# Kernel optimization log

Measured on AMD Instinct MI355X. Metric: run time of the kernel, lower is better.

## Reference

```python
import jax, jax.numpy as jnp
import numpy as np

HEADS = 8
HEAD_DIM = 64
GROUPS = 32
EPS = 1e-5


def setup_inputs() -> dict:
    key = jax.random.key(0)
    ks = jax.random.split(key, 8)
    B, C, H, W = 16, 256, 32, 32
    TD = 1024
    inner = HEADS * HEAD_DIM
    return {
        "x": jax.random.normal(ks[0], (B, C, H, W), jnp.float32),
        "embedding": jax.random.normal(ks[1], (B, TD), jnp.float32),
        "norm_w": jnp.ones((C,), jnp.float32),
        "norm_b": jnp.zeros((C,), jnp.float32),
        "in_w": jax.random.normal(ks[2], (3 * inner, C), jnp.float32) * (1.0 / np.sqrt(C)),
        "in_b": jnp.zeros((3 * inner,), jnp.float32),
        "out_w": jax.random.normal(ks[3], (C, inner), jnp.float32) * (1.0 / np.sqrt(inner)),
        "out_b": jnp.zeros((C,), jnp.float32),
        "emb_w": jax.random.normal(ks[4], (C, TD), jnp.float32) * (1.0 / np.sqrt(TD)),
        "emb_b": jnp.zeros((C,), jnp.float32),
    }


def reference(x, embedding, norm_w, norm_b, in_w, in_b, out_w, out_b, emb_w, emb_b):
    b, c, h, w = x.shape
    scale = 1.0 / np.sqrt(HEAD_DIM)
    # GroupNorm over (C//G, H, W) per group
    xg = x.reshape(b, GROUPS, -1)
    mean = xg.mean(-1, keepdims=True)
    var = xg.var(-1, keepdims=True)
    xn = ((xg - mean) * jax.lax.rsqrt(var + EPS)).reshape(b, c, h, w)
    xn = xn * norm_w[:, None, None] + norm_b[:, None, None]
    # 1x1 conv QKV projection: [b, 3*inner, h, w]
    qkv = jnp.einsum('oc,bchw->bohw', in_w, xn) + in_b[:, None, None]
    q, k, v = jnp.split(qkv, 3, axis=1)
    # [b, heads, head_dim, hw]
    q = q.reshape(b, HEADS, HEAD_DIM, h * w)
    k = k.reshape(b, HEADS, HEAD_DIM, h * w)
    v = v.reshape(b, HEADS, HEAD_DIM, h * w)
    attn = jax.nn.softmax(jnp.einsum('bhcm,bhcn->bhmn', q, k) * scale, axis=-1)
    o = jnp.einsum('bhmn,bhcn->bhcm', attn, v)  # [b,h,c,hw]
    o = o.reshape(b, HEADS * HEAD_DIM, h, w)
    out = jnp.einsum('oc,bchw->bohw', out_w, o) + out_b[:, None, None]
    emb = embedding @ emb_w.T + emb_b  # [b, C]
    return out * emb[:, :, None, None] + x
```

## Files before the change

### kernel.cpp

```cpp
#include <hip/hip_runtime.h>

#define DEV __device__ __forceinline__

typedef _Float16 f16;
typedef _Float16 f16x8 __attribute__((ext_vector_type(8)));
typedef _Float16 f16x4 __attribute__((ext_vector_type(4)));
typedef float f32x4 __attribute__((ext_vector_type(4)));

static constexpr int NB = 16;
static constexpr int NC = 256;
static constexpr int HW = 1024;
static constexpr int NG = 32;
static constexpr int CPG = 8;
static constexpr int NH = 8;
static constexpr int HD = 64;
static constexpr int INNER = 512;
static constexpr int TD = 1024;

DEV f32x4 mfma16(f16x8 a, f16x8 b, f32x4 c) {
    return __builtin_amdgcn_mfma_f32_16x16x32_f16(a, b, c, 0, 0, 0);
}

__global__ void gn_stats_k(const float* __restrict__ x, float* __restrict__ stats) {
    int bg = blockIdx.x;
    const float4* p = reinterpret_cast<const float4*>(x) + (size_t)bg * (CPG * HW / 4);
    float s = 0.f, ss = 0.f;
    for (int i = threadIdx.x; i < CPG * HW / 4; i += 256) {
        float4 v = p[i];
        s  += v.x + v.y + v.z + v.w;
        ss += v.x * v.x + v.y * v.y + v.z * v.z + v.w * v.w;
    }
    #pragma unroll
    for (int o = 32; o > 0; o >>= 1) {
        s  += __shfl_xor(s, o);
        ss += __shfl_xor(ss, o);
    }
    __shared__ float rs[4], rss[4];
    int wid = threadIdx.x >> 6;
    if ((threadIdx.x & 63) == 0) { rs[wid] = s; rss[wid] = ss; }
    __syncthreads();
    if (threadIdx.x == 0) {
        s  = rs[0] + rs[1] + rs[2] + rs[3];
        ss = rss[0] + rss[1] + rss[2] + rss[3];
        const float inv_n = 1.f / (float)(CPG * HW);
        float mean = s * inv_n;
        float var  = ss * inv_n - mean * mean;
        stats[bg * 2]     = mean;
        stats[bg * 2 + 1] = rsqrtf(var + 1e-5f);
    }
}

__global__ void gn_apply_k(const float* __restrict__ x, const float* __restrict__ stats,
                           const float* __restrict__ nw, const float* __restrict__ nb,
                           f16* __restrict__ xnT) {
    int b = blockIdx.y;
    int m = blockIdx.x * 256 + threadIdx.x;
    const float* xb = x + (size_t)b * NC * HW + m;
    f16* op = xnT + ((size_t)b * HW + m) * NC;
    for (int c0 = 0; c0 < NC; c0 += 4) {
        f16x4 h;
        #pragma unroll
        for (int j = 0; j < 4; ++j) {
            int c = c0 + j;
            float mean = stats[(b * NG + (c >> 3)) * 2];
            float rstd = stats[(b * NG + (c >> 3)) * 2 + 1];
            float v = xb[(size_t)c * HW];
            h[j] = (f16)(((v - mean) * rstd) * nw[c] + nb[c]);
        }
        *reinterpret_cast<f16x4*>(op + c0) = h;
    }
}

__global__ void conv_w_k(const float* __restrict__ a, const float* __restrict__ bw,
                         f16* __restrict__ wa, f16* __restrict__ wb) {
    int i = blockIdx.x * 256 + threadIdx.x;
    const int N1 = 3 * INNER * NC / 4;
    float4 v;
    f16* dst;
    if (i < N1) { v = reinterpret_cast<const float4*>(a)[i];      dst = wa + (size_t)i * 4; }
    else        { v = reinterpret_cast<const float4*>(bw)[i - N1]; dst = wb + (size_t)(i - N1) * 4; }
    f16x4 h4 = {(f16)v.x, (f16)v.y, (f16)v.z, (f16)v.w};
    *reinterpret_cast<f16x4*>(dst) = h4;
}

__global__ __launch_bounds__(256) void gemm_qkv_k(
        const f16* __restrict__ wA, const f16* __restrict__ xnT,
        const float* __restrict__ bias,
        f16* __restrict__ qT, f16* __restrict__ kT, f16* __restrict__ vv) {
    int b  = blockIdx.z;
    int o0 = blockIdx.x * 128;
    int m0 = blockIdx.y * 128;
    int wid  = threadIdx.x >> 6;
    int lane = threadIdx.x & 63;
    int wr = (wid >> 1) * 64, wc = (wid & 1) * 64;
    int lr = lane & 15, lg = lane >> 4;

    const f16* A  = wA  + (size_t)(o0 + wr + lr) * NC + lg * 8;
    const f16* Bp = xnT + ((size_t)b * HW + m0 + wc + lr) * NC + lg * 8;

    const f32x4 fzero = {0.f, 0.f, 0.f, 0.f};
    f32x4 acc[4][4];
    #pragma unroll
    for (int i = 0; i < 4; ++i) {
        #pragma unroll
        for (int j = 0; j < 4; ++j) acc[i][j] = fzero;
    }

    for (int k0 = 0; k0 < NC; k0 += 32) {
        f16x8 af[4], bf[4];
        #pragma unroll
        for (int i = 0; i < 4; ++i)
            af[i] = *reinterpret_cast<const f16x8*>(A + (size_t)i * 16 * NC + k0);
        #pragma unroll
        for (int j = 0; j < 4; ++j)
            bf[j] = *reinterpret_cast<const f16x8*>(Bp + (size_t)j * 16 * NC + k0);
        #pragma unroll
        for (int i = 0; i < 4; ++i) {
            #pragma unroll
            for (int j = 0; j < 4; ++j)
                acc[i][j] = mfma16(af[i], bf[j], acc[i][j]);
        }
    }

    #pragma unroll
    for (int i = 0; i < 4; ++i) {
        int ob = o0 + wr + i * 16 + lg * 4;
        #pragma unroll
        for (int j = 0; j < 4; ++j) {
            int m = m0 + wc + j * 16 + lr;
            float v0 = acc[i][j][0] + bias[ob];
            float v1 = acc[i][j][1] + bias[ob + 1];
            float v2 = acc[i][j][2] + bias[ob + 2];
            float v3 = acc[i][j][3] + bias[ob + 3];
            if (ob < INNER) {
                int h = ob >> 6, c = ob & 63;
                f16x4 pk = {(f16)v0, (f16)v1, (f16)v2, (f16)v3};
                *reinterpret_cast<f16x4*>(qT + (((size_t)(b * NH + h) * HW + m) * HD + c)) = pk;
            } else if (ob < 2 * INNER) {
                int oo = ob - INNER;
                int h = oo >> 6, c = oo & 63;
                f16x4 pk = {(f16)v0, (f16)v1, (f16)v2, (f16)v3};
                *reinterpret_cast<f16x4*>(kT + (((size_t)(b * NH + h) * HW + m) * HD + c)) = pk;
            } else {
                int oo = ob - 2 * INNER;
                int h = oo >> 6, c = oo & 63;
                f16* vp = vv + ((size_t)(b * NH + h) * HD + c) * HW + m;
                vp[0]      = (f16)v0;
                vp[HW]     = (f16)v1;
                vp[2 * HW] = (f16)v2;
                vp[3 * HW] = (f16)v3;
            }
        }
    }
}

__global__ void emb_gemm_k(const float* __restrict__ e, const float* __restrict__ ew,
                           const float* __restrict__ eb, float* __restrict__ embS) {
    int b = blockIdx.y;
    int co = blockIdx.x * 4 + (threadIdx.x >> 6);
    int lane = threadIdx.x & 63;
    const float4* ep = reinterpret_cast<const float4*>(e + (size_t)b * TD);
    const float4* wp = reinterpret_cast<const float4*>(ew + (size_t)co * TD);
    float s = 0.f;
    for (int t = lane; t < TD / 4; t += 64) {
        float4 a = ep[t], w = wp[t];
        s += a.x * w.x + a.y * w.y + a.z * w.z + a.w * w.w;
    }
    #pragma unroll
    for (int o = 32; o > 0; o >>= 1) s += __shfl_xor(s, o);
    if (lane == 0) embS[b * NC + co] = s + eb[co];
}

__global__ __launch_bounds__(256) void attn_k(
        const f16* __restrict__ qT, const f16* __restrict__ kT, const f16* __restrict__ vv,
        f16* __restrict__ oT) {
    int bh = blockIdx.x;
    int b = bh >> 3, h = bh & 7;
    int wid = threadIdx.x >> 6;
    int lane = threadIdx.x & 63;
    int lr = lane & 15, lg = lane >> 4;
    int mw = blockIdx.y * 256 + wid * 64;

    const f16* qp = qT + (size_t)bh * HW * HD;
    const f16* kp = kT + (size_t)bh * HW * HD;
    const f16* vp = vv + (size_t)bh * HD * HW;

    const float sl = 0.125f * 1.44269504088896f;

    __shared__ __align__(16) f16 pl[4][16][40];

    f16x8 qf[4][2];
    #pragma unroll
    for (int qt = 0; qt < 4; ++qt)
        #pragma unroll
        for (int ks2 = 0; ks2 < 2; ++ks2)
            qf[qt][ks2] = *reinterpret_cast<const f16x8*>(
                qp + (size_t)(mw + qt * 16 + lr) * HD + ks2 * 32 + lg * 8);

    const f32x4 fzero = {0.f, 0.f, 0.f, 0.f};
    f32x4 oa[4][4];
    #pragma unroll
    for (int qt = 0; qt < 4; ++qt)
        #pragma unroll
        for (int dt = 0; dt < 4; ++dt) oa[qt][dt] = fzero;
    float mr[4] = {-1e30f, -1e30f, -1e30f, -1e30f};
    float ls[4] = {0.f, 0.f, 0.f, 0.f};

    for (int n0 = 0; n0 < HW; n0 += 32) {
        f16x8 kf[2][2];
        #pragma unroll
        for (int kt = 0; kt < 2; ++kt)
            #pragma unroll
            for (int ks2 = 0; ks2 < 2; ++ks2)
                kf[kt][ks2] = *reinterpret_cast<const f16x8*>(
                    kp + (size_t)(n0 + kt * 16 + lr) * HD + ks2 * 32 + lg * 8);
        f16x8 vf[4];
        #pragma unroll
        for (int dt = 0; dt < 4; ++dt)
            vf[dt] = *reinterpret_cast<const f16x8*>(
                vp + (size_t)(dt * 16 + lr) * HW + n0 + lg * 8);

        #pragma unroll
        for (int qt = 0; qt < 4; ++qt) {
            f32x4 sc[2] = {fzero, fzero};
            __builtin_amdgcn_s_setprio(1);
            #pragma unroll
            for (int kt = 0; kt < 2; ++kt)
                #pragma unroll
                for (int ks2 = 0; ks2 < 2; ++ks2)
                    sc[kt] = mfma16(kf[kt][ks2], qf[qt][ks2], sc[kt]);
            __builtin_amdgcn_s_setprio(0);

            float a0 = fmaxf(fmaxf(sc[0][0], sc[0][1]), fmaxf(sc[0][2], sc[0][3]));
            float a1 = fmaxf(fmaxf(sc[1][0], sc[1][1]), fmaxf(sc[1][2], sc[1][3]));
            float pm = fmaxf(a0, a1) * sl;
            pm = fmaxf(pm, __shfl_xor(pm, 16));
            pm = fmaxf(pm, __shfl_xor(pm, 32));
            float mn = fmaxf(mr[qt], pm);
            float f = exp2f(mr[qt] - mn);
            mr[qt] = mn;
            ls[qt] *= f;
            #pragma unroll
            for (int dt = 0; dt < 4; ++dt) {
                #pragma unroll
                for (int r = 0; r < 4; ++r) oa[qt][dt][r] *= f;
            }
            float p[8];
            #pragma unroll
            for (int kt = 0; kt < 2; ++kt)
                #pragma unroll
                for (int r = 0; r < 4; ++r)
                    p[kt * 4 + r] = exp2f(fmaf(sc[kt][r], sl, -mn));
            float rsum = ((p[0] + p[1]) + (p[2] + p[3])) + ((p[4] + p[5]) + (p[6] + p[7]));
            rsum += __shfl_xor(rsum, 16);
            rsum += __shfl_xor(rsum, 32);
            ls[qt] += rsum;

            f16x4 w0 = {(f16)p[0], (f16)p[1], (f16)p[2], (f16)p[3]};
            f16x4 w1 = {(f16)p[4], (f16)p[5], (f16)p[6], (f16)p[7]};
            *reinterpret_cast<f16x4*>(&pl[wid][lr][lg * 4])      = w0;
            *reinterpret_cast<f16x4*>(&pl[wid][lr][16 + lg * 4]) = w1;
            f16x8 pf = *reinterpret_cast<const f16x8*>(&pl[wid][lr][lg * 8]);

            __builtin_amdgcn_s_setprio(1);
            #pragma unroll
            for (int dt = 0; dt < 4; ++dt)
                oa[qt][dt] = mfma16(vf[dt], pf, oa[qt][dt]);
            __builtin_amdgcn_s_setprio(0);
        }
    }

    #pragma unroll
    for (int qt = 0; qt < 4; ++qt) {
        float inv = 1.f / ls[qt];
        int m = mw + qt * 16 + lr;
        f16* op = oT + ((size_t)b * HW + m) * INNER + h * HD;
        #pragma unroll
        for (int dt = 0; dt < 4; ++dt) {
            f16x4 o4;
            #pragma unroll
            for (int r = 0; r < 4; ++r) o4[r] = (f16)(oa[qt][dt][r] * inv);
            *reinterpret_cast<f16x4*>(op + dt * 16 + lg * 4) = o4;
        }
    }
}

__global__ __launch_bounds__(256) void gemm_out_k(
        const f16* __restrict__ wA, const f16* __restrict__ oT,
        const float* __restrict__ bias, const float* __restrict__ embS,
        const float* __restrict__ x, float* __restrict__ out) {
    int b  = blockIdx.z;
    int o0 = blockIdx.x * 128;
    int m0 = blockIdx.y * 128;
    int wid  = threadIdx.x >> 6;
    int lane = threadIdx.x & 63;
    int wr = (wid >> 1) * 64, wc = (wid & 1) * 64;
    int lr = lane & 15, lg = lane >> 4;

    const f16* A  = wA + (size_t)(o0 + wr + lr) * INNER + lg * 8;
    const f16* Bp = oT + ((size_t)b * HW + m0 + wc + lr) * INNER + lg * 8;

    const f32x4 fzero = {0.f, 0.f, 0.f, 0.f};
    f32x4 acc[4][4];
    #pragma unroll
    for (int i = 0; i < 4; ++i) {
        #pragma unroll
        for (int j = 0; j < 4; ++j) acc[i][j] = fzero;
    }

    for (int k0 = 0; k0 < INNER; k0 += 32) {
        f16x8 af[4], bf[4];
        #pragma unroll
        for (int i = 0; i < 4; ++i)
            af[i] = *reinterpret_cast<const f16x8*>(A + (size_t)i * 16 * INNER + k0);
        #pragma unroll
        for (int j = 0; j < 4; ++j)
            bf[j] = *reinterpret_cast<const f16x8*>(Bp + (size_t)j * 16 * INNER + k0);
        #pragma unroll
        for (int i = 0; i < 4; ++i) {
            #pragma unroll
            for (int j = 0; j < 4; ++j)
                acc[i][j] = mfma16(af[i], bf[j], acc[i][j]);
        }
    }

    #pragma unroll
    for (int i = 0; i < 4; ++i) {
        int ob = o0 + wr + i * 16 + lg * 4;
        #pragma unroll
        for (int j = 0; j < 4; ++j) {
            int m = m0 + wc + j * 16 + lr;
            #pragma unroll
            for (int r = 0; r < 4; ++r) {
                int o = ob + r;
                size_t idx = ((size_t)b * NC + o) * HW + m;
                out[idx] = (acc[i][j][r] + bias[o]) * embS[b * NC + o] + x[idx];
            }
        }
    }
}

extern "C" void kernel_launch(void* const* d_in, const int* in_sizes, int n_in,
                              void* d_out, int out_size, void* d_ws, size_t ws_size,
                              hipStream_t stream) {
    const float* x     = (const float*)d_in[0];
    const float* emb   = (const float*)d_in[1];
    const float* nw    = (const float*)d_in[2];
    const float* nbi   = (const float*)d_in[3];
    const float* in_w  = (const float*)d_in[4];
    const float* in_b  = (const float*)d_in[5];
    const float* out_w = (const float*)d_in[6];
    const float* out_b = (const float*)d_in[7];
    const float* emb_w = (const float*)d_in[8];
    const float* emb_b = (const float*)d_in[9];

    char* p = (char*)d_ws;
    f16* xnT   = (f16*)p;   p += (size_t)NB * HW * NC * 2;
    f16* w_in  = (f16*)p;   p += (size_t)3 * INNER * NC * 2;
    f16* w_out = (f16*)p;   p += (size_t)NC * INNER * 2;
    float* stats = (float*)p; p += (size_t)NB * NG * 2 * 4;
    float* embS  = (float*)p; p += (size_t)NB * NC * 4;
    f16* qT = (f16*)p;      p += (size_t)NB * NH * HW * HD * 2;
    f16* kT = (f16*)p;      p += (size_t)NB * NH * HW * HD * 2;
    f16* vv = (f16*)p;      p += (size_t)NB * NH * HW * HD * 2;
    f16* oT = (f16*)p;

    gn_stats_k<<<NB * NG, 256, 0, stream>>>(x, stats);
    gn_apply_k<<<dim3(HW / 256, NB), 256, 0, stream>>>(x, stats, nw, nbi, xnT);
    conv_w_k<<<512, 256, 0, stream>>>(in_w, out_w, w_in, w_out);
    gemm_qkv_k<<<dim3(12, 8, NB), 256, 0, stream>>>(w_in, xnT, in_b, qT, kT, vv);
    emb_gemm_k<<<dim3(NC / 4, NB), 256, 0, stream>>>(emb, emb_w, emb_b, embS);
    attn_k<<<dim3(NB * NH, HW / 256), 256, 0, stream>>>(qT, kT, vv, oT);
    gemm_out_k<<<dim3(NC / 128, HW / 128, NB), 256, 0, stream>>>(w_out, oT, out_b, embS, x, (float*)d_out);
}
```

Before: 197.2 us.

## Double-buffer K/V loads, lazy softmax rescale, per-lane row sums, XCD-aware block mapping

```diff
diff --git a/kernel.cpp b/kernel.cpp
--- a/kernel.cpp
+++ b/kernel.cpp
@@ -171,108 +171,124 @@
     if (lane == 0) embS[b * NC + co] = s + eb[co];
 }
 
-__global__ __launch_bounds__(256) void attn_k(
-        const f16* __restrict__ qT, const f16* __restrict__ kT, const f16* __restrict__ vv,
-        f16* __restrict__ oT) {
-    int bh = blockIdx.x;
-    int b = bh >> 3, h = bh & 7;
-    int wid = threadIdx.x >> 6;
-    int lane = threadIdx.x & 63;
-    int lr = lane & 15, lg = lane >> 4;
-    int mw = blockIdx.y * 256 + wid * 64;
-
-    const f16* qp = qT + (size_t)bh * HW * HD;
-    const f16* kp = kT + (size_t)bh * HW * HD;
-    const f16* vp = vv + (size_t)bh * HD * HW;
-
+DEV void load_kv(const f16* __restrict__ kp, const f16* __restrict__ vp,
+                 int n0, int lr, int lg, f16x8 (&kf)[2][2], f16x8 (&vf)[4]) {
+    #pragma unroll
+    for (int kt = 0; kt < 2; ++kt)
+        #pragma unroll
+        for (int ks2 = 0; ks2 < 2; ++ks2)
+            kf[kt][ks2] = *reinterpret_cast<const f16x8*>(
+                kp + (size_t)(n0 + kt * 16 + lr) * HD + ks2 * 32 + lg * 8);
+    #pragma unroll
+    for (int dt = 0; dt < 4; ++dt)
+        vf[dt] = *reinterpret_cast<const f16x8*>(
+            vp + (size_t)(dt * 16 + lr) * HW + n0 + lg * 8);
+}
+
+DEV void attn_tile(const f16x8 (&kf)[2][2], const f16x8 (&vf)[4],
+                   const f16x8 (&qf)[4][2],
+                   f32x4 (&oa)[4][4], float (&mr)[4], float (&lsl)[4],
+                   f16 (&pl)[16][40], int lr, int lg) {
     const float sl = 0.125f * 1.44269504088896f;
-
-    __shared__ __align__(16) f16 pl[4][16][40];
-
-    f16x8 qf[4][2];
-    #pragma unroll
-    for (int qt = 0; qt < 4; ++qt)
-        #pragma unroll
-        for (int ks2 = 0; ks2 < 2; ++ks2)
-            qf[qt][ks2] = *reinterpret_cast<const f16x8*>(
-                qp + (size_t)(mw + qt * 16 + lr) * HD + ks2 * 32 + lg * 8);
-
+    const float THR = 11.0f;
     const f32x4 fzero = {0.f, 0.f, 0.f, 0.f};
-    f32x4 oa[4][4];
-    #pragma unroll
-    for (int qt = 0; qt < 4; ++qt)
-        #pragma unroll
-        for (int dt = 0; dt < 4; ++dt) oa[qt][dt] = fzero;
-    float mr[4] = {-1e30f, -1e30f, -1e30f, -1e30f};
-    float ls[4] = {0.f, 0.f, 0.f, 0.f};
-
-    for (int n0 = 0; n0 < HW; n0 += 32) {
-        f16x8 kf[2][2];
-        #pragma unroll
-        for (int kt = 0; kt < 2; ++kt)
-            #pragma unroll
-            for (int ks2 = 0; ks2 < 2; ++ks2)
-                kf[kt][ks2] = *reinterpret_cast<const f16x8*>(
-                    kp + (size_t)(n0 + kt * 16 + lr) * HD + ks2 * 32 + lg * 8);
-        f16x8 vf[4];
-        #pragma unroll
-        for (int dt = 0; dt < 4; ++dt)
-            vf[dt] = *reinterpret_cast<const f16x8*>(
-                vp + (size_t)(dt * 16 + lr) * HW + n0 + lg * 8);
-
-        #pragma unroll
-        for (int qt = 0; qt < 4; ++qt) {
-            f32x4 sc[2] = {fzero, fzero};
-            __builtin_amdgcn_s_setprio(1);
-            #pragma unroll
-            for (int kt = 0; kt < 2; ++kt)
-                #pragma unroll
-                for (int ks2 = 0; ks2 < 2; ++ks2)
-                    sc[kt] = mfma16(kf[kt][ks2], qf[qt][ks2], sc[kt]);
-            __builtin_amdgcn_s_setprio(0);
-
-            float a0 = fmaxf(fmaxf(sc[0][0], sc[0][1]), fmaxf(sc[0][2], sc[0][3]));
-            float a1 = fmaxf(fmaxf(sc[1][0], sc[1][1]), fmaxf(sc[1][2], sc[1][3]));
-            float pm = fmaxf(a0, a1) * sl;
+    #pragma unroll
+    for (int qt = 0; qt < 4; ++qt) {
+        f32x4 sc0 = fzero, sc1 = fzero;
+        __builtin_amdgcn_s_setprio(1);
+        sc0 = mfma16(kf[0][0], qf[qt][0], sc0);
+        sc0 = mfma16(kf[0][1], qf[qt][1], sc0);
+        sc1 = mfma16(kf[1][0], qf[qt][0], sc1);
+        sc1 = mfma16(kf[1][1], qf[qt][1], sc1);
+        __builtin_amdgcn_s_setprio(0);
+
+        float a0 = fmaxf(fmaxf(sc0[0], sc0[1]), fmaxf(sc0[2], sc0[3]));
+        float a1 = fmaxf(fmaxf(sc1[0], sc1[1]), fmaxf(sc1[2], sc1[3]));
+        float pmax = fmaxf(a0, a1) * sl;
+        if (__any(pmax - mr[qt] > THR)) {
+            float pm = pmax;
             pm = fmaxf(pm, __shfl_xor(pm, 16));
             pm = fmaxf(pm, __shfl_xor(pm, 32));
             float mn = fmaxf(mr[qt], pm);
             float f = exp2f(mr[qt] - mn);
             mr[qt] = mn;
-            ls[qt] *= f;
-            #pragma unroll
-            for (int dt = 0; dt < 4; ++dt) {
+            lsl[qt] *= f;
+            #pragma unroll
+            for (int dt = 0; dt < 4; ++dt)
                 #pragma unroll
                 for (int r = 0; r < 4; ++r) oa[qt][dt][r] *= f;
-            }
-            float p[8];
-            #pragma unroll
-            for (int kt = 0; kt < 2; ++kt)
-                #pragma unroll
-                for (int r = 0; r < 4; ++r)
-                    p[kt * 4 + r] = exp2f(fmaf(sc[kt][r], sl, -mn));
-            float rsum = ((p[0] + p[1]) + (p[2] + p[3])) + ((p[4] + p[5]) + (p[6] + p[7]));
-            rsum += __shfl_xor(rsum, 16);
-            rsum += __shfl_xor(rsum, 32);
-            ls[qt] += rsum;
-
-            f16x4 w0 = {(f16)p[0], (f16)p[1], (f16)p[2], (f16)p[3]};
-            f16x4 w1 = {(f16)p[4], (f16)p[5], (f16)p[6], (f16)p[7]};
-            *reinterpret_cast<f16x4*>(&pl[wid][lr][lg * 4])      = w0;
-            *reinterpret_cast<f16x4*>(&pl[wid][lr][16 + lg * 4]) = w1;
-            f16x8 pf = *reinterpret_cast<const f16x8*>(&pl[wid][lr][lg * 8]);
-
-            __builtin_amdgcn_s_setprio(1);
-            #pragma unroll
-            for (int dt = 0; dt < 4; ++dt)
-                oa[qt][dt] = mfma16(vf[dt], pf, oa[qt][dt]);
-            __builtin_amdgcn_s_setprio(0);
-        }
+        }
+        float p[8];
+        #pragma unroll
+        for (int r = 0; r < 4; ++r) p[r]     = exp2f(fmaf(sc0[r], sl, -mr[qt]));
+        #pragma unroll
+        for (int r = 0; r < 4; ++r) p[4 + r] = exp2f(fmaf(sc1[r], sl, -mr[qt]));
+        lsl[qt] += ((p[0] + p[1]) + (p[2] + p[3])) + ((p[4] + p[5]) + (p[6] + p[7]));
+
+        f16x4 w0 = {(f16)p[0], (f16)p[1], (f16)p[2], (f16)p[3]};
+        f16x4 w1 = {(f16)p[4], (f16)p[5], (f16)p[6], (f16)p[7]};
+        *reinterpret_cast<f16x4*>(&pl[lr][lg * 4])      = w0;
+        *reinterpret_cast<f16x4*>(&pl[lr][16 + lg * 4]) = w1;
+        f16x8 pf = *reinterpret_cast<const f16x8*>(&pl[lr][lg * 8]);
+
+        __builtin_amdgcn_s_setprio(1);
+        #pragma unroll
+        for (int dt = 0; dt < 4; ++dt)
+            oa[qt][dt] = mfma16(vf[dt], pf, oa[qt][dt]);
+        __builtin_amdgcn_s_setprio(0);
+    }
+}
+
+__global__ __launch_bounds__(256) void attn_k(
+        const f16* __restrict__ qT, const f16* __restrict__ kT, const f16* __restrict__ vv,
+        f16* __restrict__ oT) {
+    int u = ((blockIdx.x & 7) << 6) | (blockIdx.x >> 3);
+    int bh = u >> 2;
+    int mt = u & 3;
+    int b = bh >> 3, h = bh & 7;
+    int wid = threadIdx.x >> 6;
+    int lane = threadIdx.x & 63;
+    int lr = lane & 15, lg = lane >> 4;
+    int mw = mt * 256 + wid * 64;
+
+    const f16* qp = qT + (size_t)bh * HW * HD;
+    const f16* kp = kT + (size_t)bh * HW * HD;
+    const f16* vp = vv + (size_t)bh * HD * HW;
+
+    __shared__ __align__(16) f16 pl[4][16][40];
+
+    f16x8 qf[4][2];
+    #pragma unroll
+    for (int qt = 0; qt < 4; ++qt)
+        #pragma unroll
+        for (int ks2 = 0; ks2 < 2; ++ks2)
+            qf[qt][ks2] = *reinterpret_cast<const f16x8*>(
+                qp + (size_t)(mw + qt * 16 + lr) * HD + ks2 * 32 + lg * 8);
+
+    const f32x4 fzero = {0.f, 0.f, 0.f, 0.f};
+    f32x4 oa[4][4];
+    #pragma unroll
+    for (int qt = 0; qt < 4; ++qt)
+        #pragma unroll
+        for (int dt = 0; dt < 4; ++dt) oa[qt][dt] = fzero;
+    float mr[4]  = {-1e30f, -1e30f, -1e30f, -1e30f};
+    float lsl[4] = {0.f, 0.f, 0.f, 0.f};
+
+    f16x8 kfA[2][2], vfA[4], kfB[2][2], vfB[4];
+    load_kv(kp, vp, 0, lr, lg, kfA, vfA);
+    for (int n0 = 0; n0 < HW; n0 += 64) {
+        load_kv(kp, vp, n0 + 32, lr, lg, kfB, vfB);
+        attn_tile(kfA, vfA, qf, oa, mr, lsl, pl[wid], lr, lg);
+        if (n0 + 64 < HW) load_kv(kp, vp, n0 + 64, lr, lg, kfA, vfA);
+        attn_tile(kfB, vfB, qf, oa, mr, lsl, pl[wid], lr, lg);
     }
 
     #pragma unroll
     for (int qt = 0; qt < 4; ++qt) {
-        float inv = 1.f / ls[qt];
+        float t = lsl[qt];
+        t += __shfl_xor(t, 16);
+        t += __shfl_xor(t, 32);
+        float inv = 1.f / t;
         int m = mw + qt * 16 + lr;
         f16* op = oT + ((size_t)b * HW + m) * INNER + h * HD;
         #pragma unroll
@@ -370,6 +386,6 @@
     conv_w_k<<<512, 256, 0, stream>>>(in_w, out_w, w_in, w_out);
     gemm_qkv_k<<<dim3(12, 8, NB), 256, 0, stream>>>(w_in, xnT, in_b, qT, kT, vv);
     emb_gemm_k<<<dim3(NC / 4, NB), 256, 0, stream>>>(emb, emb_w, emb_b, embS);
-    attn_k<<<dim3(NB * NH, HW / 256), 256, 0, stream>>>(qT, kT, vv, oT);
+    attn_k<<<512, 256, 0, stream>>>(qT, kT, vv, oT);
     gemm_out_k<<<dim3(NC / 128, HW / 128, NB), 256, 0, stream>>>(w_out, oT, out_b, embS, x, (float*)d_out);
 }
```

Measured after the change: 178.4 us. -9.5%, faster.
